# Optimization experiments

Hardware: AMD Instinct MI355X
Metric: run time of the kernel (lower is better)

Reference implementation:

```python
import jax, jax.numpy as jnp
import numpy as np

NUM_SEQ, NUM_RES = 512, 768
MSA_C, PAIR_C, NUM_HEAD = 64, 128, 8
VALUE_DIM = MSA_C // NUM_HEAD
EPS = 1e-5


def _layernorm(x, scale, bias):
    mu = jnp.mean(x, axis=-1, keepdims=True)
    var = jnp.var(x, axis=-1, keepdims=True)
    return (x - mu) * jax.lax.rsqrt(var + EPS) * scale + bias


def setup_inputs() -> dict:
    key = jax.random.key(0)
    ks = jax.random.split(key, 8)
    act = jax.random.normal(ks[0], (NUM_SEQ, NUM_RES, MSA_C), dtype=jnp.float32)
    mask = jnp.ones((NUM_SEQ, NUM_RES), dtype=jnp.float32)
    pair_act = jax.random.normal(ks[1], (NUM_RES, NUM_RES, PAIR_C), dtype=jnp.float32)
    # learned params
    act_scale = jnp.ones((MSA_C,), jnp.float32)
    act_bias = jnp.zeros((MSA_C,), jnp.float32)
    pair_scale = jnp.ones((PAIR_C,), jnp.float32)
    pair_bias = jnp.zeros((PAIR_C,), jnp.float32)
    w_pair_logits = jax.random.normal(ks[2], (NUM_HEAD, PAIR_C), jnp.float32) * (PAIR_C ** -0.5)
    v_proj = jax.random.normal(ks[3], (MSA_C, NUM_HEAD, VALUE_DIM), jnp.float32) * (MSA_C ** -0.5)
    w_gate = jax.random.normal(ks[4], (MSA_C, MSA_C), jnp.float32) * (MSA_C ** -0.5)
    w_out = jax.random.normal(ks[5], (MSA_C, MSA_C), jnp.float32) * (MSA_C ** -0.5)
    return {
        "act": act, "mask": mask, "pair_act": pair_act,
        "act_scale": act_scale, "act_bias": act_bias,
        "pair_scale": pair_scale, "pair_bias": pair_bias,
        "w_pair_logits": w_pair_logits, "v_proj": v_proj,
        "w_gate": w_gate, "w_out": w_out,
    }


def reference(act, mask, pair_act, act_scale, act_bias, pair_scale, pair_bias,
              w_pair_logits, v_proj, w_gate, w_out):
    act = _layernorm(act, act_scale, act_bias)            # [b, k, i]
    pair = _layernorm(pair_act, pair_scale, pair_bias)    # [q, k, c]
    logits = jnp.einsum('qkc,hc->hqk', pair, w_pair_logits)  # [h, q, k]
    # mask reduced over MSA rows; torch casts to bf16 before the bias add
    mask_max = jnp.max(mask, axis=0).astype(jnp.bfloat16)    # [k]
    logits = logits + 1e9 * (mask_max.astype(logits.dtype) - 1.0)
    weights = jax.nn.softmax(logits, axis=-1)                # [h, q, k]
    v = jnp.einsum('bki,ihc->bkhc', act, v_proj)             # [b, k, h, c]
    v_avg = jnp.einsum('hqk,bkhc->bqhc', weights, v)         # [b, q, h, c]
    v_avg = v_avg.reshape(v_avg.shape[0], v_avg.shape[1], -1)  # [b, q, h*c]
    gate = jax.nn.sigmoid(act @ w_gate.T)
    return (v_avg * gate) @ w_out.T
```

## Files before the change

kernel.cpp:

```cpp
#include <hip/hip_runtime.h>
#include <hip/hip_bf16.h>

#define NSEQ 512
#define NRES 768
#define MSAC 64
#define PAIRC 128
#define NHEAD 8

typedef __attribute__((ext_vector_type(8))) short short8_t;
typedef __attribute__((ext_vector_type(4))) float f32x4;

__device__ __forceinline__ float bf2f(unsigned short u){
  return __uint_as_float(((unsigned int)u) << 16);
}
__device__ __forceinline__ unsigned short f2bf(float f){
  unsigned int x = __float_as_uint(f);
  x += 0x7fffu + ((x >> 16) & 1u);
  return (unsigned short)(x >> 16);
}
__device__ __forceinline__ void glds16(const void* g, void* l){
  __builtin_amdgcn_global_load_lds(
      (const __attribute__((address_space(1))) unsigned int*)g,
      (__attribute__((address_space(3))) unsigned int*)l, 16, 0, 0);
}

__global__ __launch_bounds__(256) void k_prep2(
    const float* __restrict__ mask, const float* __restrict__ vproj,
    const float* __restrict__ wgate, const float* __restrict__ wout,
    float* __restrict__ bias, unsigned short* __restrict__ WvT,
    unsigned short* __restrict__ WgT, unsigned short* __restrict__ WoH,
    unsigned short* __restrict__ WoL)
{
  const int bid = blockIdx.x, tid = threadIdx.x;
  if (bid < 12){
    __shared__ float red[4][64];
    const int kk = bid*64 + (tid & 63);
    const int bs = tid >> 6;
    float m = -1e30f;
    for (int b = bs; b < NSEQ; b += 4) m = fmaxf(m, mask[(size_t)b*NRES + kk]);
    red[bs][tid & 63] = m;
    __syncthreads();
    if (tid < 64){
      float mm = fmaxf(fmaxf(red[0][tid], red[1][tid]),
                       fmaxf(red[2][tid], red[3][tid]));
      bias[bid*64 + tid] = 1e9f * (bf2f(f2bf(mm)) - 1.0f);
    }
  } else {
    const int t = (bid - 12)*256 + tid;
    const int j = t >> 6, i = t & 63;
    WvT[t] = f2bf(vproj[i*64 + j]);
    WgT[t] = f2bf(wgate[t]);
    float wv = wout[t];
    unsigned short hh = f2bf(wv);
    WoH[t] = hh;
    WoL[t] = f2bf(wv - bf2f(hh));
  }
}

__global__ __launch_bounds__(256) void k_pair(
    const float* __restrict__ pair, const float* __restrict__ pscale,
    const float* __restrict__ pbias, const float* __restrict__ wl,
    const float* __restrict__ mbias, unsigned short* __restrict__ weights)
{
  __shared__ float lg[NHEAD][NRES];
  const int q = blockIdx.x;
  const int tid = threadIdx.x;
  const int wv = tid >> 6, lane = tid & 63;
  const int g = lane & 7;
  const int c0 = g * 16;

  float scl[16], bsl[16];
  #pragma unroll
  for (int i = 0; i < 4; ++i){
    float4 s4 = *(const float4*)(pscale + c0 + i*4);
    float4 b4 = *(const float4*)(pbias  + c0 + i*4);
    scl[4*i+0]=s4.x; scl[4*i+1]=s4.y; scl[4*i+2]=s4.z; scl[4*i+3]=s4.w;
    bsl[4*i+0]=b4.x; bsl[4*i+1]=b4.y; bsl[4*i+2]=b4.z; bsl[4*i+3]=b4.w;
  }
  unsigned int wp[8][8];
  #pragma unroll
  for (int h = 0; h < 8; ++h){
    #pragma unroll
    for (int jj = 0; jj < 8; ++jj){
      float2 w2 = *(const float2*)(wl + h*PAIRC + c0 + jj*2);
      wp[h][jj] = (unsigned int)f2bf(w2.x) | ((unsigned int)f2bf(w2.y) << 16);
    }
  }

  for (int it = 0; it < 24; ++it){
    int k = it*32 + wv*8 + (lane >> 3);
    const float* prow = pair + ((size_t)q * NRES + k) * PAIRC + c0;
    float x[16];
    #pragma unroll
    for (int i = 0; i < 4; ++i){
      float4 v4 = *(const float4*)(prow + i*4);
      x[4*i+0]=v4.x; x[4*i+1]=v4.y; x[4*i+2]=v4.z; x[4*i+3]=v4.w;
    }
    float s = 0.f, ss = 0.f;
    #pragma unroll
    for (int i = 0; i < 16; ++i){ s += x[i]; ss += x[i]*x[i]; }
    #pragma unroll
    for (int m = 1; m < 8; m <<= 1){
      s  += __shfl_xor(s,  m, 64);
      ss += __shfl_xor(ss, m, 64);
    }
    float mu  = s * (1.f/128.f);
    float var = ss * (1.f/128.f) - mu*mu;
    float rs  = rsqrtf(var + 1e-5f);
    #pragma unroll
    for (int i = 0; i < 16; ++i) x[i] = (x[i] - mu) * rs * scl[i] + bsl[i];
    float ph[8];
    #pragma unroll
    for (int h = 0; h < 8; ++h){
      float p = 0.f;
      #pragma unroll
      for (int jj = 0; jj < 8; ++jj){
        unsigned int w = wp[h][jj];
        float wlo = __uint_as_float(w << 16);
        float whi = __uint_as_float(w & 0xffff0000u);
        p += x[2*jj] * wlo + x[2*jj+1] * whi;
      }
      ph[h] = p;
    }
    #pragma unroll
    for (int h = 0; h < 8; ++h){
      #pragma unroll
      for (int m = 1; m < 8; m <<= 1) ph[h] += __shfl_xor(ph[h], m, 64);
    }
    #pragma unroll
    for (int h = 0; h < 8; ++h) if (g == h) lg[h][k] = ph[h];
  }
  __syncthreads();
  #pragma unroll
  for (int hh = 0; hh < 2; ++hh){
    int h = wv + hh*4;
    float mx = -1e30f;
    for (int kk = lane; kk < NRES; kk += 64) mx = fmaxf(mx, lg[h][kk] + mbias[kk]);
    #pragma unroll
    for (int m = 1; m < 64; m <<= 1) mx = fmaxf(mx, __shfl_xor(mx, m, 64));
    float sum = 0.f;
    for (int kk = lane; kk < NRES; kk += 64){
      float e = __expf(lg[h][kk] + mbias[kk] - mx);
      lg[h][kk] = e; sum += e;
    }
    #pragma unroll
    for (int m = 1; m < 64; m <<= 1) sum += __shfl_xor(sum, m, 64);
    float inv = 1.0f / sum;
    unsigned short* wrow = weights + ((size_t)h * NRES + q) * NRES;
    for (int kk = lane; kk < NRES; kk += 64) wrow[kk] = f2bf(lg[h][kk] * inv);
  }
}

__global__ __launch_bounds__(256) void k_act(
    const float* __restrict__ act, const float* __restrict__ ascale,
    const float* __restrict__ abias, const unsigned short* __restrict__ WvT,
    const unsigned short* __restrict__ WgT, unsigned short* __restrict__ v,
    unsigned short* __restrict__ gate)
{
  __shared__ unsigned short vt[64][72];
  __shared__ unsigned short gt[64][72];
  const int b  = blockIdx.x / 12;
  const int k0 = (blockIdx.x % 12) * 64;
  const int tid = threadIdx.x, w = tid >> 6, lane = tid & 63;
  const int lr = lane & 15;
  const int lc = lane >> 4;
  const int row = k0 + w*16 + lr;

  const float* arow = act + ((size_t)b*NRES + row)*MSAC;
  float x[2][8];
  #pragma unroll
  for (int s = 0; s < 2; ++s){
    float4 t0 = *(const float4*)(arow + s*32 + lc*8);
    float4 t1 = *(const float4*)(arow + s*32 + lc*8 + 4);
    x[s][0]=t0.x; x[s][1]=t0.y; x[s][2]=t0.z; x[s][3]=t0.w;
    x[s][4]=t1.x; x[s][5]=t1.y; x[s][6]=t1.z; x[s][7]=t1.w;
  }
  float ps = 0.f, pss = 0.f;
  #pragma unroll
  for (int s = 0; s < 2; ++s)
    #pragma unroll
    for (int e = 0; e < 8; ++e){ ps += x[s][e]; pss += x[s][e]*x[s][e]; }
  ps  += __shfl_xor(ps, 16, 64);  pss += __shfl_xor(pss, 16, 64);
  ps  += __shfl_xor(ps, 32, 64);  pss += __shfl_xor(pss, 32, 64);
  const float mu  = ps * (1.f/64.f);
  const float var = pss * (1.f/64.f) - mu*mu;
  const float rs  = rsqrtf(var + 1e-5f);

  short8_t a[2];
  #pragma unroll
  for (int s = 0; s < 2; ++s){
    float4 s0 = *(const float4*)(ascale + s*32 + lc*8);
    float4 s1 = *(const float4*)(ascale + s*32 + lc*8 + 4);
    float4 b0 = *(const float4*)(abias  + s*32 + lc*8);
    float4 b1 = *(const float4*)(abias  + s*32 + lc*8 + 4);
    const float sc[8] = {s0.x,s0.y,s0.z,s0.w,s1.x,s1.y,s1.z,s1.w};
    const float bs[8] = {b0.x,b0.y,b0.z,b0.w,b1.x,b1.y,b1.z,b1.w};
    #pragma unroll
    for (int e = 0; e < 8; ++e)
      a[s][e] = (short)f2bf((x[s][e] - mu)*rs*sc[e] + bs[e]);
  }

  short8_t bv[4][2], bg[4][2];
  #pragma unroll
  for (int mf = 0; mf < 4; ++mf){
    #pragma unroll
    for (int s = 0; s < 2; ++s){
      bv[mf][s] = *(const short8_t*)(WvT + (mf*16 + lr)*64 + s*32 + lc*8);
      bg[mf][s] = *(const short8_t*)(WgT + (mf*16 + lr)*64 + s*32 + lc*8);
    }
  }

  f32x4 accv[4], accg[4];
  #pragma unroll
  for (int mf = 0; mf < 4; ++mf){ accv[mf] = 0.f; accg[mf] = 0.f; }
  #pragma unroll
  for (int mf = 0; mf < 4; ++mf){
    #pragma unroll
    for (int s = 0; s < 2; ++s){
      accv[mf] = __builtin_amdgcn_mfma_f32_16x16x32_bf16(a[s], bv[mf][s], accv[mf], 0, 0, 0);
      accg[mf] = __builtin_amdgcn_mfma_f32_16x16x32_bf16(bg[mf][s], a[s], accg[mf], 0, 0, 0);
    }
  }

  #pragma unroll
  for (int mf = 0; mf < 4; ++mf){
    ushort4 ov;
    ov.x = f2bf(accv[mf][0]); ov.y = f2bf(accv[mf][1]);
    ov.z = f2bf(accv[mf][2]); ov.w = f2bf(accv[mf][3]);
    *(ushort4*)&vt[mf*16 + lr][w*16 + lc*4] = ov;
    ushort4 og;
    og.x = f2bf(1.0f/(1.0f + __expf(-accg[mf][0])));
    og.y = f2bf(1.0f/(1.0f + __expf(-accg[mf][1])));
    og.z = f2bf(1.0f/(1.0f + __expf(-accg[mf][2])));
    og.w = f2bf(1.0f/(1.0f + __expf(-accg[mf][3])));
    *(ushort4*)&gt[w*16 + lr][mf*16 + lc*4] = og;
  }
  __syncthreads();
  #pragma unroll
  for (int it = 0; it < 2; ++it){
    int fl = it*256 + tid;
    int j = fl >> 3, chunk = fl & 7;
    uint4 val = *(const uint4*)&vt[j][chunk*8];
    *(uint4*)(v + ((size_t)(j >> 3)*4096 + (size_t)b*8 + (j & 7))*NRES + k0 + chunk*8) = val;
  }
  #pragma unroll
  for (int it = 0; it < 2; ++it){
    int fl = it*256 + tid;
    int k = fl >> 3, chunk = fl & 7;
    uint4 val = *(const uint4*)&gt[k][chunk*8];
    *(uint4*)(gate + ((size_t)b*NRES + k0 + k)*MSAC + chunk*8) = val;
  }
}

__global__ __launch_bounds__(256) void k_wavg(
    const unsigned short* __restrict__ V, const unsigned short* __restrict__ W,
    unsigned short* __restrict__ Y)
{
  __shared__ unsigned char smem[32768];

  const int flat = blockIdx.x;
  const int nid  = (flat & 7) * 192 + (flat >> 3);
  const int m    = nid % 192;
  const int by   = m % 6;
  const int bx   = m / 6;
  const int h    = nid / 192;

  const int tid = threadIdx.x, wid = tid >> 6, lane = tid & 63;
  const int wm = wid & 1, wn = wid >> 1;
  const unsigned short* Ag = V + (size_t)h*4096*768 + (size_t)bx*128*768;
  const unsigned short* Bg = W + (size_t)h*768*768 + (size_t)by*128*768;

  f32x4 acc[4][4];
  #pragma unroll
  for (int i=0;i<4;++i){
    #pragma unroll
    for (int jj=0;jj<4;++jj) acc[i][jj] = 0.f;
  }

  #define STAGE_K(bufsel, kt) { \
    unsigned char* Ab = smem + (bufsel)*16384; \
    unsigned char* Bb = Ab + 8192; \
    _Pragma("unroll") \
    for (int r = 0; r < 2; ++r){ \
      int cid = tid + r*256; \
      int rw = cid >> 2, ch = cid & 3; \
      int sc = ch ^ ((rw >> 1) & 3); \
      glds16(Ag + (size_t)rw*768 + (kt)*32 + sc*8, Ab + cid*16 - lane*16); \
      glds16(Bg + (size_t)rw*768 + (kt)*32 + sc*8, Bb + cid*16 - lane*16); \
    } }

  STAGE_K(0, 0);
  __syncthreads();
  const int c0 = lane >> 4;
  for (int kt = 0; kt < 24; ++kt){
    if (kt < 23) STAGE_K((kt+1)&1, kt+1);
    unsigned char* Ab = smem + (kt&1)*16384;
    unsigned char* Bb = Ab + 8192;
    short8_t af[4], bf[4];
    #pragma unroll
    for (int mf = 0; mf < 4; ++mf){
      int row = wm*64 + mf*16 + (lane & 15);
      int off = row*64 + ((c0 ^ ((row>>1)&3)) << 4);
      af[mf] = *(const short8_t*)(Ab + off);
    }
    #pragma unroll
    for (int nf = 0; nf < 4; ++nf){
      int row = wn*64 + nf*16 + (lane & 15);
      int off = row*64 + ((c0 ^ ((row>>1)&3)) << 4);
      bf[nf] = *(const short8_t*)(Bb + off);
    }
    #pragma unroll
    for (int mf = 0; mf < 4; ++mf){
      #pragma unroll
      for (int nf = 0; nf < 4; ++nf)
        acc[mf][nf] = __builtin_amdgcn_mfma_f32_16x16x32_bf16(af[mf], bf[nf], acc[mf][nf], 0, 0, 0);
    }
    __syncthreads();
  }
  #undef STAGE_K

  unsigned char* Ds = smem;
  #pragma unroll
  for (int mf = 0; mf < 4; ++mf){
    int bc = wm*64 + mf*16 + ((lane >> 4) << 2);
    #pragma unroll
    for (int nf = 0; nf < 4; ++nf){
      int q = wn*64 + nf*16 + (lane & 15);
      f32x4 a = acc[mf][nf];
      ushort4 o;
      o.x = f2bf(a[0]); o.y = f2bf(a[1]); o.z = f2bf(a[2]); o.w = f2bf(a[3]);
      int off = q*256 + bc*2; off ^= (q & 7) << 4;
      *(ushort4*)(Ds + off) = o;
    }
  }
  __syncthreads();
  unsigned short* Yb = Y + ((size_t)(h*32 + bx)*768 + by*128)*128;
  #pragma unroll
  for (int it = 0; it < 8; ++it){
    int fl = it*256 + tid;
    int q = fl >> 4, chunk = fl & 15;
    int off = q*256 + chunk*16; off ^= (q & 7) << 4;
    uint4 val = *(const uint4*)(Ds + off);
    *(uint4*)(Yb + (size_t)fl*8) = val;
  }
}

__global__ __launch_bounds__(256) void k_final(
    const unsigned short* __restrict__ Y, const unsigned short* __restrict__ gate,
    const unsigned short* __restrict__ WoH, const unsigned short* __restrict__ WoL,
    float* __restrict__ out)
{
  const int b  = blockIdx.x & 511;
  const int q0 = (blockIdx.x >> 9) * 64;
  const int tid = threadIdx.x, w = tid >> 6, lane = tid & 63;
  const int lr = lane & 15, lc = lane >> 4;

  short8_t bh[4][2], bl[4][2];
  #pragma unroll
  for (int nf = 0; nf < 4; ++nf){
    #pragma unroll
    for (int s = 0; s < 2; ++s){
      bh[nf][s] = *(const short8_t*)(WoH + (nf*16 + lr)*64 + s*32 + lc*8);
      bl[nf][s] = *(const short8_t*)(WoL + (nf*16 + lr)*64 + s*32 + lc*8);
    }
  }

  const int q = q0 + w*16 + lr;
  short8_t ah[2], al[2];
  #pragma unroll
  for (int s = 0; s < 2; ++s){
    const int hh = s*4 + lc;
    short8_t y8 = *(const short8_t*)(Y + ((size_t)(hh*32 + (b >> 4))*768 + q)*128 + (b & 15)*8);
    short8_t g8 = *(const short8_t*)(gate + ((size_t)b*NRES + q)*MSAC + s*32 + lc*8);
    #pragma unroll
    for (int e = 0; e < 8; ++e){
      float p = bf2f((unsigned short)y8[e]) * bf2f((unsigned short)g8[e]);
      unsigned short hi = f2bf(p);
      ah[s][e] = (short)hi;
      al[s][e] = (short)f2bf(p - bf2f(hi));
    }
  }

  f32x4 acc[4];
  #pragma unroll
  for (int nf = 0; nf < 4; ++nf) acc[nf] = 0.f;
  #pragma unroll
  for (int nf = 0; nf < 4; ++nf){
    #pragma unroll
    for (int s = 0; s < 2; ++s){
      acc[nf] = __builtin_amdgcn_mfma_f32_16x16x32_bf16(ah[s], bh[nf][s], acc[nf], 0, 0, 0);
      acc[nf] = __builtin_amdgcn_mfma_f32_16x16x32_bf16(al[s], bh[nf][s], acc[nf], 0, 0, 0);
      acc[nf] = __builtin_amdgcn_mfma_f32_16x16x32_bf16(ah[s], bl[nf][s], acc[nf], 0, 0, 0);
    }
  }

  #pragma unroll
  for (int nf = 0; nf < 4; ++nf){
    #pragma unroll
    for (int e = 0; e < 4; ++e){
      int qq = q0 + w*16 + lc*4 + e;
      out[((size_t)b*NRES + qq)*MSAC + nf*16 + lr] = acc[nf][e];
    }
  }
}

extern "C" void kernel_launch(void* const* d_in, const int* in_sizes, int n_in,
                              void* d_out, int out_size, void* d_ws, size_t ws_size,
                              hipStream_t stream) {
  (void)in_sizes; (void)n_in; (void)out_size; (void)ws_size;
  const float* act    = (const float*)d_in[0];
  const float* mask   = (const float*)d_in[1];
  const float* pair   = (const float*)d_in[2];
  const float* ascale = (const float*)d_in[3];
  const float* abias  = (const float*)d_in[4];
  const float* pscale = (const float*)d_in[5];
  const float* pbias  = (const float*)d_in[6];
  const float* wl     = (const float*)d_in[7];
  const float* vproj  = (const float*)d_in[8];
  const float* wgate  = (const float*)d_in[9];
  const float* wout   = (const float*)d_in[10];
  float* out = (float*)d_out;

  char* ws = (char*)d_ws;
  float*          mbias   = (float*)(ws);
  unsigned short* WvT     = (unsigned short*)(ws + 4096);
  unsigned short* WgT     = (unsigned short*)(ws + 12288);
  unsigned short* WoH     = (unsigned short*)(ws + 20480);
  unsigned short* WoL     = (unsigned short*)(ws + 28672);
  unsigned short* weights = (unsigned short*)(ws + 36864);
  unsigned short* v       = (unsigned short*)(ws + 36864 + 9437184);
  unsigned short* gate    = (unsigned short*)(ws + 36864 + 9437184 + 50331648);
  unsigned short* y       = (unsigned short*)(ws + 36864 + 9437184 + 2*50331648ull);

  k_prep2<<<dim3(28), dim3(256), 0, stream>>>(mask, vproj, wgate, wout,
                                              mbias, WvT, WgT, WoH, WoL);
  k_pair<<<dim3(768), dim3(256), 0, stream>>>(pair, pscale, pbias, wl, mbias, weights);
  k_act<<<dim3(6144), dim3(256), 0, stream>>>(act, ascale, abias, WvT, WgT, v, gate);
  k_wavg<<<dim3(1536), dim3(256), 0, stream>>>(v, weights, y);
  k_final<<<dim3(6144), dim3(256), 0, stream>>>(y, gate, WoH, WoL, out);
}
```

Before: 358.3 us.

## Merge pair-logits and act-projection kernels into one launch; remap k_final block order

The pair-logit/softmax kernel and the act LayerNorm/projection kernel are merged into one launch whose blocks branch on block index, so the two independent stages can run concurrently on the GPU instead of back to back. This removes one launch boundary and the tail idle time of the 768-block pair kernel. Shared memory is unified into one 24KB buffer, which may lower occupancy for the act blocks. k_final's block-to-(b,q) mapping is also permuted to change the order in which Y and gate are read.

```diff
diff --git a/kernel.cpp b/kernel.cpp
--- a/kernel.cpp
+++ b/kernel.cpp
@@ -57,198 +57,201 @@
   }
 }
 
-__global__ __launch_bounds__(256) void k_pair(
+__global__ __launch_bounds__(256) void k_pairact(
     const float* __restrict__ pair, const float* __restrict__ pscale,
     const float* __restrict__ pbias, const float* __restrict__ wl,
-    const float* __restrict__ mbias, unsigned short* __restrict__ weights)
-{
-  __shared__ float lg[NHEAD][NRES];
-  const int q = blockIdx.x;
-  const int tid = threadIdx.x;
-  const int wv = tid >> 6, lane = tid & 63;
-  const int g = lane & 7;
-  const int c0 = g * 16;
-
-  float scl[16], bsl[16];
-  #pragma unroll
-  for (int i = 0; i < 4; ++i){
-    float4 s4 = *(const float4*)(pscale + c0 + i*4);
-    float4 b4 = *(const float4*)(pbias  + c0 + i*4);
-    scl[4*i+0]=s4.x; scl[4*i+1]=s4.y; scl[4*i+2]=s4.z; scl[4*i+3]=s4.w;
-    bsl[4*i+0]=b4.x; bsl[4*i+1]=b4.y; bsl[4*i+2]=b4.z; bsl[4*i+3]=b4.w;
-  }
-  unsigned int wp[8][8];
-  #pragma unroll
-  for (int h = 0; h < 8; ++h){
-    #pragma unroll
-    for (int jj = 0; jj < 8; ++jj){
-      float2 w2 = *(const float2*)(wl + h*PAIRC + c0 + jj*2);
-      wp[h][jj] = (unsigned int)f2bf(w2.x) | ((unsigned int)f2bf(w2.y) << 16);
-    }
-  }
-
-  for (int it = 0; it < 24; ++it){
-    int k = it*32 + wv*8 + (lane >> 3);
-    const float* prow = pair + ((size_t)q * NRES + k) * PAIRC + c0;
-    float x[16];
-    #pragma unroll
-    for (int i = 0; i < 4; ++i){
-      float4 v4 = *(const float4*)(prow + i*4);
-      x[4*i+0]=v4.x; x[4*i+1]=v4.y; x[4*i+2]=v4.z; x[4*i+3]=v4.w;
-    }
-    float s = 0.f, ss = 0.f;
-    #pragma unroll
-    for (int i = 0; i < 16; ++i){ s += x[i]; ss += x[i]*x[i]; }
-    #pragma unroll
-    for (int m = 1; m < 8; m <<= 1){
-      s  += __shfl_xor(s,  m, 64);
-      ss += __shfl_xor(ss, m, 64);
-    }
-    float mu  = s * (1.f/128.f);
-    float var = ss * (1.f/128.f) - mu*mu;
-    float rs  = rsqrtf(var + 1e-5f);
-    #pragma unroll
-    for (int i = 0; i < 16; ++i) x[i] = (x[i] - mu) * rs * scl[i] + bsl[i];
-    float ph[8];
-    #pragma unroll
-    for (int h = 0; h < 8; ++h){
-      float p = 0.f;
-      #pragma unroll
-      for (int jj = 0; jj < 8; ++jj){
-        unsigned int w = wp[h][jj];
-        float wlo = __uint_as_float(w << 16);
-        float whi = __uint_as_float(w & 0xffff0000u);
-        p += x[2*jj] * wlo + x[2*jj+1] * whi;
-      }
-      ph[h] = p;
-    }
-    #pragma unroll
-    for (int h = 0; h < 8; ++h){
-      #pragma unroll
-      for (int m = 1; m < 8; m <<= 1) ph[h] += __shfl_xor(ph[h], m, 64);
-    }
-    #pragma unroll
-    for (int h = 0; h < 8; ++h) if (g == h) lg[h][k] = ph[h];
-  }
-  __syncthreads();
-  #pragma unroll
-  for (int hh = 0; hh < 2; ++hh){
-    int h = wv + hh*4;
-    float mx = -1e30f;
-    for (int kk = lane; kk < NRES; kk += 64) mx = fmaxf(mx, lg[h][kk] + mbias[kk]);
-    #pragma unroll
-    for (int m = 1; m < 64; m <<= 1) mx = fmaxf(mx, __shfl_xor(mx, m, 64));
-    float sum = 0.f;
-    for (int kk = lane; kk < NRES; kk += 64){
-      float e = __expf(lg[h][kk] + mbias[kk] - mx);
-      lg[h][kk] = e; sum += e;
-    }
-    #pragma unroll
-    for (int m = 1; m < 64; m <<= 1) sum += __shfl_xor(sum, m, 64);
-    float inv = 1.0f / sum;
-    unsigned short* wrow = weights + ((size_t)h * NRES + q) * NRES;
-    for (int kk = lane; kk < NRES; kk += 64) wrow[kk] = f2bf(lg[h][kk] * inv);
-  }
-}
-
-__global__ __launch_bounds__(256) void k_act(
+    const float* __restrict__ mbias, unsigned short* __restrict__ weights,
     const float* __restrict__ act, const float* __restrict__ ascale,
     const float* __restrict__ abias, const unsigned short* __restrict__ WvT,
     const unsigned short* __restrict__ WgT, unsigned short* __restrict__ v,
     unsigned short* __restrict__ gate)
 {
-  __shared__ unsigned short vt[64][72];
-  __shared__ unsigned short gt[64][72];
-  const int b  = blockIdx.x / 12;
-  const int k0 = (blockIdx.x % 12) * 64;
-  const int tid = threadIdx.x, w = tid >> 6, lane = tid & 63;
-  const int lr = lane & 15;
-  const int lc = lane >> 4;
-  const int row = k0 + w*16 + lr;
-
-  const float* arow = act + ((size_t)b*NRES + row)*MSAC;
-  float x[2][8];
-  #pragma unroll
-  for (int s = 0; s < 2; ++s){
-    float4 t0 = *(const float4*)(arow + s*32 + lc*8);
-    float4 t1 = *(const float4*)(arow + s*32 + lc*8 + 4);
-    x[s][0]=t0.x; x[s][1]=t0.y; x[s][2]=t0.z; x[s][3]=t0.w;
-    x[s][4]=t1.x; x[s][5]=t1.y; x[s][6]=t1.z; x[s][7]=t1.w;
-  }
-  float ps = 0.f, pss = 0.f;
-  #pragma unroll
-  for (int s = 0; s < 2; ++s)
-    #pragma unroll
-    for (int e = 0; e < 8; ++e){ ps += x[s][e]; pss += x[s][e]*x[s][e]; }
-  ps  += __shfl_xor(ps, 16, 64);  pss += __shfl_xor(pss, 16, 64);
-  ps  += __shfl_xor(ps, 32, 64);  pss += __shfl_xor(pss, 32, 64);
-  const float mu  = ps * (1.f/64.f);
-  const float var = pss * (1.f/64.f) - mu*mu;
-  const float rs  = rsqrtf(var + 1e-5f);
-
-  short8_t a[2];
-  #pragma unroll
-  for (int s = 0; s < 2; ++s){
-    float4 s0 = *(const float4*)(ascale + s*32 + lc*8);
-    float4 s1 = *(const float4*)(ascale + s*32 + lc*8 + 4);
-    float4 b0 = *(const float4*)(abias  + s*32 + lc*8);
-    float4 b1 = *(const float4*)(abias  + s*32 + lc*8 + 4);
-    const float sc[8] = {s0.x,s0.y,s0.z,s0.w,s1.x,s1.y,s1.z,s1.w};
-    const float bs[8] = {b0.x,b0.y,b0.z,b0.w,b1.x,b1.y,b1.z,b1.w};
-    #pragma unroll
-    for (int e = 0; e < 8; ++e)
-      a[s][e] = (short)f2bf((x[s][e] - mu)*rs*sc[e] + bs[e]);
-  }
-
-  short8_t bv[4][2], bg[4][2];
-  #pragma unroll
-  for (int mf = 0; mf < 4; ++mf){
+  __shared__ __align__(16) unsigned char sm[24576];
+  const int bid = blockIdx.x;
+  const int tid = threadIdx.x;
+
+  if (bid < 768){
+    float (*lg)[NRES] = (float (*)[NRES])sm;
+    const int q = bid;
+    const int wv = tid >> 6, lane = tid & 63;
+    const int g = lane & 7;
+    const int c0 = g * 16;
+
+    float scl[16], bsl[16];
+    #pragma unroll
+    for (int i = 0; i < 4; ++i){
+      float4 s4 = *(const float4*)(pscale + c0 + i*4);
+      float4 b4 = *(const float4*)(pbias  + c0 + i*4);
+      scl[4*i+0]=s4.x; scl[4*i+1]=s4.y; scl[4*i+2]=s4.z; scl[4*i+3]=s4.w;
+      bsl[4*i+0]=b4.x; bsl[4*i+1]=b4.y; bsl[4*i+2]=b4.z; bsl[4*i+3]=b4.w;
+    }
+    unsigned int wp[8][8];
+    #pragma unroll
+    for (int h = 0; h < 8; ++h){
+      #pragma unroll
+      for (int jj = 0; jj < 8; ++jj){
+        float2 w2 = *(const float2*)(wl + h*PAIRC + c0 + jj*2);
+        wp[h][jj] = (unsigned int)f2bf(w2.x) | ((unsigned int)f2bf(w2.y) << 16);
+      }
+    }
+
+    for (int it = 0; it < 24; ++it){
+      int k = it*32 + wv*8 + (lane >> 3);
+      const float* prow = pair + ((size_t)q * NRES + k) * PAIRC + c0;
+      float x[16];
+      #pragma unroll
+      for (int i = 0; i < 4; ++i){
+        float4 v4 = *(const float4*)(prow + i*4);
+        x[4*i+0]=v4.x; x[4*i+1]=v4.y; x[4*i+2]=v4.z; x[4*i+3]=v4.w;
+      }
+      float s = 0.f, ss = 0.f;
+      #pragma unroll
+      for (int i = 0; i < 16; ++i){ s += x[i]; ss += x[i]*x[i]; }
+      #pragma unroll
+      for (int m = 1; m < 8; m <<= 1){
+        s  += __shfl_xor(s,  m, 64);
+        ss += __shfl_xor(ss, m, 64);
+      }
+      float mu  = s * (1.f/128.f);
+      float var = ss * (1.f/128.f) - mu*mu;
+      float rs  = rsqrtf(var + 1e-5f);
+      #pragma unroll
+      for (int i = 0; i < 16; ++i) x[i] = (x[i] - mu) * rs * scl[i] + bsl[i];
+      float ph[8];
+      #pragma unroll
+      for (int h = 0; h < 8; ++h){
+        float p = 0.f;
+        #pragma unroll
+        for (int jj = 0; jj < 8; ++jj){
+          unsigned int w = wp[h][jj];
+          float wlo = __uint_as_float(w << 16);
+          float whi = __uint_as_float(w & 0xffff0000u);
+          p += x[2*jj] * wlo + x[2*jj+1] * whi;
+        }
+        ph[h] = p;
+      }
+      #pragma unroll
+      for (int h = 0; h < 8; ++h){
+        #pragma unroll
+        for (int m = 1; m < 8; m <<= 1) ph[h] += __shfl_xor(ph[h], m, 64);
+      }
+      #pragma unroll
+      for (int h = 0; h < 8; ++h) if (g == h) lg[h][k] = ph[h];
+    }
+    __syncthreads();
+    #pragma unroll
+    for (int hh = 0; hh < 2; ++hh){
+      int h = wv + hh*4;
+      float mx = -1e30f;
+      for (int kk = lane; kk < NRES; kk += 64) mx = fmaxf(mx, lg[h][kk] + mbias[kk]);
+      #pragma unroll
+      for (int m = 1; m < 64; m <<= 1) mx = fmaxf(mx, __shfl_xor(mx, m, 64));
+      float sum = 0.f;
+      for (int kk = lane; kk < NRES; kk += 64){
+        float e = __expf(lg[h][kk] + mbias[kk] - mx);
+        lg[h][kk] = e; sum += e;
+      }
+      #pragma unroll
+      for (int m = 1; m < 64; m <<= 1) sum += __shfl_xor(sum, m, 64);
+      float inv = 1.0f / sum;
+      unsigned short* wrow = weights + ((size_t)h * NRES + q) * NRES;
+      for (int kk = lane; kk < NRES; kk += 64) wrow[kk] = f2bf(lg[h][kk] * inv);
+    }
+  } else {
+    unsigned short (*vt)[72] = (unsigned short (*)[72])sm;
+    unsigned short (*gt)[72] = (unsigned short (*)[72])(sm + 9216);
+    const int abid = bid - 768;
+    const int b  = abid / 12;
+    const int k0 = (abid % 12) * 64;
+    const int w = tid >> 6, lane = tid & 63;
+    const int lr = lane & 15;
+    const int lc = lane >> 4;
+    const int row = k0 + w*16 + lr;
+
+    const float* arow = act + ((size_t)b*NRES + row)*MSAC;
+    float x[2][8];
     #pragma unroll
     for (int s = 0; s < 2; ++s){
-      bv[mf][s] = *(const short8_t*)(WvT + (mf*16 + lr)*64 + s*32 + lc*8);
-      bg[mf][s] = *(const short8_t*)(WgT + (mf*16 + lr)*64 + s*32 + lc*8);
-    }
-  }
-
-  f32x4 accv[4], accg[4];
-  #pragma unroll
-  for (int mf = 0; mf < 4; ++mf){ accv[mf] = 0.f; accg[mf] = 0.f; }
-  #pragma unroll
-  for (int mf = 0; mf < 4; ++mf){
+      float4 t0 = *(const float4*)(arow + s*32 + lc*8);
+      float4 t1 = *(const float4*)(arow + s*32 + lc*8 + 4);
+      x[s][0]=t0.x; x[s][1]=t0.y; x[s][2]=t0.z; x[s][3]=t0.w;
+      x[s][4]=t1.x; x[s][5]=t1.y; x[s][6]=t1.z; x[s][7]=t1.w;
+    }
+    float ps = 0.f, pss = 0.f;
+    #pragma unroll
+    for (int s = 0; s < 2; ++s)
+      #pragma unroll
+      for (int e = 0; e < 8; ++e){ ps += x[s][e]; pss += x[s][e]*x[s][e]; }
+    ps  += __shfl_xor(ps, 16, 64);  pss += __shfl_xor(pss, 16, 64);
+    ps  += __shfl_xor(ps, 32, 64);  pss += __shfl_xor(pss, 32, 64);
+    const float mu  = ps * (1.f/64.f);
+    const float var = pss * (1.f/64.f) - mu*mu;
+    const float rs  = rsqrtf(var + 1e-5f);
+
+    short8_t a[2];
     #pragma unroll
     for (int s = 0; s < 2; ++s){
-      accv[mf] = __builtin_amdgcn_mfma_f32_16x16x32_bf16(a[s], bv[mf][s], accv[mf], 0, 0, 0);
-      accg[mf] = __builtin_amdgcn_mfma_f32_16x16x32_bf16(bg[mf][s], a[s], accg[mf], 0, 0, 0);
-    }
-  }
-
-  #pragma unroll
-  for (int mf = 0; mf < 4; ++mf){
-    ushort4 ov;
-    ov.x = f2bf(accv[mf][0]); ov.y = f2bf(accv[mf][1]);
-    ov.z = f2bf(accv[mf][2]); ov.w = f2bf(accv[mf][3]);
-    *(ushort4*)&vt[mf*16 + lr][w*16 + lc*4] = ov;
-    ushort4 og;
-    og.x = f2bf(1.0f/(1.0f + __expf(-accg[mf][0])));
-    og.y = f2bf(1.0f/(1.0f + __expf(-accg[mf][1])));
-    og.z = f2bf(1.0f/(1.0f + __expf(-accg[mf][2])));
-    og.w = f2bf(1.0f/(1.0f + __expf(-accg[mf][3])));
-    *(ushort4*)&gt[w*16 + lr][mf*16 + lc*4] = og;
-  }
-  __syncthreads();
-  #pragma unroll
-  for (int it = 0; it < 2; ++it){
-    int fl = it*256 + tid;
-    int j = fl >> 3, chunk = fl & 7;
-    uint4 val = *(const uint4*)&vt[j][chunk*8];
-    *(uint4*)(v + ((size_t)(j >> 3)*4096 + (size_t)b*8 + (j & 7))*NRES + k0 + chunk*8) = val;
-  }
-  #pragma unroll
-  for (int it = 0; it < 2; ++it){
-    int fl = it*256 + tid;
-    int k = fl >> 3, chunk = fl & 7;
-    uint4 val = *(const uint4*)&gt[k][chunk*8];
-    *(uint4*)(gate + ((size_t)b*NRES + k0 + k)*MSAC + chunk*8) = val;
+      float4 s0 = *(const float4*)(ascale + s*32 + lc*8);
+      float4 s1 = *(const float4*)(ascale + s*32 + lc*8 + 4);
+      float4 b0 = *(const float4*)(abias  + s*32 + lc*8);
+      float4 b1 = *(const float4*)(abias  + s*32 + lc*8 + 4);
+      const float sc[8] = {s0.x,s0.y,s0.z,s0.w,s1.x,s1.y,s1.z,s1.w};
+      const float bs[8] = {b0.x,b0.y,b0.z,b0.w,b1.x,b1.y,b1.z,b1.w};
+      #pragma unroll
+      for (int e = 0; e < 8; ++e)
+        a[s][e] = (short)f2bf((x[s][e] - mu)*rs*sc[e] + bs[e]);
+    }
+
+    short8_t bv[4][2], bg[4][2];
+    #pragma unroll
+    for (int mf = 0; mf < 4; ++mf){
+      #pragma unroll
+      for (int s = 0; s < 2; ++s){
+        bv[mf][s] = *(const short8_t*)(WvT + (mf*16 + lr)*64 + s*32 + lc*8);
+        bg[mf][s] = *(const short8_t*)(WgT + (mf*16 + lr)*64 + s*32 + lc*8);
+      }
+    }
+
+    f32x4 accv[4], accg[4];
+    #pragma unroll
+    for (int mf = 0; mf < 4; ++mf){ accv[mf] = 0.f; accg[mf] = 0.f; }
+    #pragma unroll
+    for (int mf = 0; mf < 4; ++mf){
+      #pragma unroll
+      for (int s = 0; s < 2; ++s){
+        accv[mf] = __builtin_amdgcn_mfma_f32_16x16x32_bf16(a[s], bv[mf][s], accv[mf], 0, 0, 0);
+        accg[mf] = __builtin_amdgcn_mfma_f32_16x16x32_bf16(bg[mf][s], a[s], accg[mf], 0, 0, 0);
+      }
+    }
+
+    #pragma unroll
+    for (int mf = 0; mf < 4; ++mf){
+      ushort4 ov;
+      ov.x = f2bf(accv[mf][0]); ov.y = f2bf(accv[mf][1]);
+      ov.z = f2bf(accv[mf][2]); ov.w = f2bf(accv[mf][3]);
+      *(ushort4*)&vt[mf*16 + lr][w*16 + lc*4] = ov;
+      ushort4 og;
+      og.x = f2bf(1.0f/(1.0f + __expf(-accg[mf][0])));
+      og.y = f2bf(1.0f/(1.0f + __expf(-accg[mf][1])));
+      og.z = f2bf(1.0f/(1.0f + __expf(-accg[mf][2])));
+      og.w = f2bf(1.0f/(1.0f + __expf(-accg[mf][3])));
+      *(ushort4*)&gt[w*16 + lr][mf*16 + lc*4] = og;
+    }
+    __syncthreads();
+    #pragma unroll
+    for (int it = 0; it < 2; ++it){
+      int fl = it*256 + tid;
+      int j = fl >> 3, chunk = fl & 7;
+      uint4 val = *(const uint4*)&vt[j][chunk*8];
+      *(uint4*)(v + ((size_t)(j >> 3)*4096 + (size_t)b*8 + (j & 7))*NRES + k0 + chunk*8) = val;
+    }
+    #pragma unroll
+    for (int it = 0; it < 2; ++it){
+      int fl = it*256 + tid;
+      int k = fl >> 3, chunk = fl & 7;
+      uint4 val = *(const uint4*)&gt[k][chunk*8];
+      *(uint4*)(gate + ((size_t)b*NRES + k0 + k)*MSAC + chunk*8) = val;
+    }
   }
 }
 
@@ -350,8 +353,10 @@
     const unsigned short* __restrict__ WoH, const unsigned short* __restrict__ WoL,
     float* __restrict__ out)
 {
-  const int b  = blockIdx.x & 511;
-  const int q0 = (blockIdx.x >> 9) * 64;
+  const int p = blockIdx.x;
+  const int r = p & 7, t = p >> 3;
+  const int b  = r*64 + (t & 63);
+  const int q0 = (t >> 6) * 64;
   const int tid = threadIdx.x, w = tid >> 6, lane = tid & 63;
   const int lr = lane & 15, lc = lane >> 4;
 
@@ -374,10 +379,10 @@
     short8_t g8 = *(const short8_t*)(gate + ((size_t)b*NRES + q)*MSAC + s*32 + lc*8);
     #pragma unroll
     for (int e = 0; e < 8; ++e){
-      float p = bf2f((unsigned short)y8[e]) * bf2f((unsigned short)g8[e]);
-      unsigned short hi = f2bf(p);
+      float pp = bf2f((unsigned short)y8[e]) * bf2f((unsigned short)g8[e]);
+      unsigned short hi = f2bf(pp);
       ah[s][e] = (short)hi;
-      al[s][e] = (short)f2bf(p - bf2f(hi));
+      al[s][e] = (short)f2bf(pp - bf2f(hi));
     }
   }
 
@@ -434,8 +439,8 @@
 
   k_prep2<<<dim3(28), dim3(256), 0, stream>>>(mask, vproj, wgate, wout,
                                               mbias, WvT, WgT, WoH, WoL);
-  k_pair<<<dim3(768), dim3(256), 0, stream>>>(pair, pscale, pbias, wl, mbias, weights);
-  k_act<<<dim3(6144), dim3(256), 0, stream>>>(act, ascale, abias, WvT, WgT, v, gate);
+  k_pairact<<<dim3(6912), dim3(256), 0, stream>>>(pair, pscale, pbias, wl, mbias, weights,
+                                                  act, ascale, abias, WvT, WgT, v, gate);
   k_wavg<<<dim3(1536), dim3(256), 0, stream>>>(v, weights, y);
   k_final<<<dim3(6144), dim3(256), 0, stream>>>(y, gate, WoH, WoL, out);
 }
```

After: 331.3 us. 1.08x faster.
